# Performance work log

Hardware: AMD Instinct MI355X
Metric: run time of the kernel (lower is better)

The kernel has to match this reference:

```python
import jax, jax.numpy as jnp
import numpy as np

N = 200000      # nodes (Elliptic-scale transaction graph)
E = 400000      # directed edges
F_IN = 165      # node features
HID = 128
OUT = 2


def setup_inputs() -> dict:
    key = jax.random.key(0)
    k = jax.random.split(key, 5)
    x = jax.random.normal(k[0], (N, F_IN), dtype=jnp.float32)
    edge_index = jax.random.randint(k[1], (2, E), 0, N, dtype=jnp.int32)
    # GCNConv params (PyG: Linear without bias semantics differ slightly by
    # version; here weight + bias, bias added after aggregation)
    W1 = jax.random.normal(k[2], (F_IN, HID), dtype=jnp.float32) * (1.0 / np.sqrt(F_IN))
    b1 = jnp.zeros((HID,), dtype=jnp.float32)
    W2 = jax.random.normal(k[3], (HID, OUT), dtype=jnp.float32) * (1.0 / np.sqrt(HID))
    b2 = jnp.zeros((OUT,), dtype=jnp.float32)
    return {"x": x, "edge_index": edge_index, "W1": W1, "b1": b1, "W2": W2, "b2": b2}


def _gcn_conv(h, edge_index, W, b):
    """PyG GCNConv: out = D^{-1/2} (A + I) D^{-1/2} (h @ W) + b."""
    h = h @ W                                    # [N, F_out]
    loop = jnp.arange(N, dtype=edge_index.dtype)
    src = jnp.concatenate([edge_index[0], loop])  # add self-loops
    dst = jnp.concatenate([edge_index[1], loop])
    # degree over destination nodes (self-loops guarantee deg >= 1)
    deg = jax.ops.segment_sum(jnp.ones_like(dst, dtype=h.dtype), dst, num_segments=N)
    dinv = jax.lax.rsqrt(deg)
    norm = dinv[src] * dinv[dst]                 # [E+N]
    msgs = h[src] * norm[:, None]                # gather + scale
    out = jax.ops.segment_sum(msgs, dst, num_segments=N)  # scatter-add
    return out + b


def reference(x, edge_index, W1, b1, W2, b2):
    h = _gcn_conv(x, edge_index, W1, b1)
    # torch.relu then F.dropout(training=False) (identity) then torch.relu:
    # in eval mode relu(relu(h)) == relu(h)
    h = jnp.maximum(h, 0.0)
    return _gcn_conv(h, edge_index, W2, b2)
```

## Files before the change

### kernel.cpp

```cpp
#include <hip/hip_runtime.h>
#include <hip/hip_bf16.h>

typedef __attribute__((ext_vector_type(8))) short bf16x8;
typedef __attribute__((ext_vector_type(4))) float f32x4;

#define N_NODES 200000
#define N_EDGES 400000
#define F_IN    165
#define HID     128
#define BM      32
#define N_TILES 6250
#define KSTEPS  6
#define PITCH   164
#define CAP     32

__device__ __forceinline__ uint bf16r(float f) {
  uint u = __float_as_uint(f);
  return (u + 0x7FFFu + ((u >> 16) & 1u)) >> 16;
}

__device__ __forceinline__ uint pkbf(float a, float b) {
  uint r;
  asm("v_cvt_pk_bf16_f32 %0, %1, %2" : "=v"(r) : "v"(a), "v"(b));
  return r;
}

__device__ __forceinline__ void gload16(const void* gp, void* lp) {
  __builtin_amdgcn_global_load_lds(
      (const __attribute__((address_space(1))) unsigned int*)gp,
      (__attribute__((address_space(3))) unsigned int*)lp, 16, 0, 0);
}


__global__ __launch_bounds__(256) void k_init(const float* __restrict__ W1,
                                              ushort* __restrict__ Wf,
                                              uint4* __restrict__ cursor) {
  int b = blockIdx.x;
  int tid = threadIdx.x;
  if (b < 96) {
    int id = b * 256 + tid;
    int j = id & 7;
    int lane = (id >> 3) & 63;
    int rem = id >> 9;
    int s = rem % 6;
    int ct = rem / 6;
    int k = s * 32 + (lane >> 4) * 8 + j;
    int col = ct * 16 + (lane & 15);
    float v = (k < F_IN) ? W1[k * HID + col] : 0.f;
    Wf[id] = (ushort)bf16r(v);
  } else {
    int i = (b - 96) * 256 + tid;
    if (i < 50000) cursor[i] = make_uint4(0, 0, 0, 0);
  }
}


__global__ __launch_bounds__(256) void k_gemm1p(const float* __restrict__ x,
                                                const ushort* __restrict__ Wf,
                                                const int* __restrict__ ei,
                                                int* __restrict__ cursor,
                                                int* __restrict__ slots,
                                                uint* __restrict__ g) {
  __shared__ float xs[BM * PITCH + BM];
  float* xe = xs + BM * PITCH;
  const int tid  = threadIdx.x;
  const int wave = tid >> 6;
  const int lane = tid & 63;
  const int r15  = lane & 15;
  const int kg   = lane >> 4;

  if (tid < 64) {
    int e = blockIdx.x * 64 + tid;
    int d = ei[N_EDGES + e];
    int pos = atomicAdd(&cursor[d], 1);
    if (pos < CAP) slots[d * CAP + pos] = ei[e];
  }

  bf16x8 bfrag[2][KSTEPS];
  #pragma unroll
  for (int t = 0; t < 2; ++t) {
    int ct = wave * 2 + t;
    #pragma unroll
    for (int s = 0; s < KSTEPS; ++s)
      bfrag[t][s] = *(const bf16x8*)(Wf + (size_t)(((ct * KSTEPS + s) * 64 + lane) << 3));
  }

  const size_t tb = (size_t)blockIdx.x * (BM * F_IN);
  #pragma unroll
  for (int it = 0; it < 5; ++it) {
    int c = it * 256 + tid;
    int row = c / 41;
    int col4 = c - row * 41;
    gload16(x + tb + (size_t)row * F_IN + col4 * 4,
            (char*)xs + (size_t)(it * 256 + wave * 64) * 16);
  }
  if (tid < 32) {
    int c = 1280 + tid;
    int row = c / 41;
    int col4 = c - row * 41;
    float4 v;
    __builtin_memcpy(&v, x + tb + (size_t)row * F_IN + col4 * 4, 16);
    *(float4*)(xs + (size_t)c * 4) = v;
    xe[tid] = x[tb + (size_t)tid * F_IN + 164];
  }
  __syncthreads();

  f32x4 acc[2][2];
  #pragma unroll
  for (int rg = 0; rg < 2; ++rg) {
    acc[rg][0] = (f32x4){0.f, 0.f, 0.f, 0.f};
    acc[rg][1] = (f32x4){0.f, 0.f, 0.f, 0.f};
  }

  #pragma unroll
  for (int rg = 0; rg < 2; ++rg) {
    const float* rp0 = xs + (rg * 16 + r15) * PITCH;
    #pragma unroll
    for (int s = 0; s < KSTEPS; ++s) {
      uint o0, o1, o2, o3;
      if (s < 5) {
        const float* rp = rp0 + s * 32 + kg * 8;
        float4 fa = *(const float4*)rp;
        float4 fb = *(const float4*)(rp + 4);
        o0 = pkbf(fa.x, fa.y);
        o1 = pkbf(fa.z, fa.w);
        o2 = pkbf(fb.x, fb.y);
        o3 = pkbf(fb.z, fb.w);
      } else {
        o0 = o1 = o2 = o3 = 0u;
        if (kg == 0) {
          float4 fa = *(const float4*)(rp0 + 160);
          float e = xe[rg * 16 + r15];
          o0 = pkbf(fa.x, fa.y);
          o1 = pkbf(fa.z, fa.w);
          o2 = pkbf(e, 0.f);
        }
      }
      uint4 uu = make_uint4(o0, o1, o2, o3);
      bf16x8 a = *(bf16x8*)&uu;
      acc[rg][0] = __builtin_amdgcn_mfma_f32_16x16x32_bf16(a, bfrag[0][s], acc[rg][0], 0, 0, 0);
      acc[rg][1] = __builtin_amdgcn_mfma_f32_16x16x32_bf16(a, bfrag[1][s], acc[rg][1], 0, 0, 0);
    }
  }

  int base = blockIdx.x * BM;
  #pragma unroll
  for (int rg = 0; rg < 2; ++rg) {
    #pragma unroll
    for (int r = 0; r < 4; ++r) {
      int row = base + rg * 16 + kg * 4 + r;
      uint u = pkbf(acc[rg][0][r], acc[rg][1][r]);
      g[(size_t)row * 64 + wave * 16 + r15] = u;
    }
  }
}


__global__ __launch_bounds__(256, 8) void k_agg1(const uint* __restrict__ g,
                                                 const int* __restrict__ cursor,
                                                 const int* __restrict__ slots,
                                                 const float* __restrict__ b1,
                                                 const float* __restrict__ W2,
                                                 float* __restrict__ g2) {
  const int tid  = threadIdx.x;
  const int lane = tid & 63;
  const int wave = tid >> 6;
  const int sub  = lane >> 4;
  const int fl   = lane & 15;
  const int node = blockIdx.x * 16 + wave * 4 + sub;

  int deg = cursor[node];
  float dv = rsqrtf(1.0f + (float)deg);
  int dcap = min(deg, 16);
  int srcl = (fl < dcap) ? slots[node * CAP + fl] : node;

  uint4 v = *(const uint4*)&g[(size_t)node * 64 + fl * 4];
  float sx0 = dv * __uint_as_float(v.x << 16), sy0 = dv * __uint_as_float(v.x & 0xFFFF0000u);
  float sx1 = dv * __uint_as_float(v.y << 16), sy1 = dv * __uint_as_float(v.y & 0xFFFF0000u);
  float sx2 = dv * __uint_as_float(v.z << 16), sy2 = dv * __uint_as_float(v.z & 0xFFFF0000u);
  float sx3 = dv * __uint_as_float(v.w << 16), sy3 = dv * __uint_as_float(v.w & 0xFFFF0000u);

  for (int j = 0; j < dcap; ++j) {
    int s = __shfl(srcl, sub * 16 + j);
    float wj = rsqrtf(1.0f + (float)cursor[s]);
    uint4 w = *(const uint4*)&g[(size_t)s * 64 + fl * 4];
    sx0 = fmaf(__uint_as_float(w.x << 16), wj, sx0);
    sy0 = fmaf(__uint_as_float(w.x & 0xFFFF0000u), wj, sy0);
    sx1 = fmaf(__uint_as_float(w.y << 16), wj, sx1);
    sy1 = fmaf(__uint_as_float(w.y & 0xFFFF0000u), wj, sy1);
    sx2 = fmaf(__uint_as_float(w.z << 16), wj, sx2);
    sy2 = fmaf(__uint_as_float(w.z & 0xFFFF0000u), wj, sy2);
    sx3 = fmaf(__uint_as_float(w.w << 16), wj, sx3);
    sy3 = fmaf(__uint_as_float(w.w & 0xFFFF0000u), wj, sy3);
  }
  for (int e = 16; e < min(deg, CAP); ++e) {
    int s = slots[node * CAP + e];
    float wj = rsqrtf(1.0f + (float)cursor[s]);
    uint4 w = *(const uint4*)&g[(size_t)s * 64 + fl * 4];
    sx0 = fmaf(__uint_as_float(w.x << 16), wj, sx0);
    sy0 = fmaf(__uint_as_float(w.x & 0xFFFF0000u), wj, sy0);
    sx1 = fmaf(__uint_as_float(w.y << 16), wj, sx1);
    sy1 = fmaf(__uint_as_float(w.y & 0xFFFF0000u), wj, sy1);
    sx2 = fmaf(__uint_as_float(w.z << 16), wj, sx2);
    sy2 = fmaf(__uint_as_float(w.z & 0xFFFF0000u), wj, sy2);
    sx3 = fmaf(__uint_as_float(w.w << 16), wj, sx3);
    sy3 = fmaf(__uint_as_float(w.w & 0xFFFF0000u), wj, sy3);
  }

  float h, p0 = 0.f, p1 = 0.f;
  #pragma unroll
  for (int k = 0; k < 4; ++k) {
    int dw = fl * 4 + k;
    int c0 = ((dw >> 4) << 5) + (dw & 15);
    float blo = b1[c0], bhi = b1[c0 + 16];
    float2 wlo = *(const float2*)&W2[c0 * 2];
    float2 whi = *(const float2*)&W2[(c0 + 16) * 2];
    float sx = (k == 0) ? sx0 : (k == 1) ? sx1 : (k == 2) ? sx2 : sx3;
    float sy = (k == 0) ? sy0 : (k == 1) ? sy1 : (k == 2) ? sy2 : sy3;
    h = fmaxf(fmaf(sx, dv, blo), 0.f); p0 = fmaf(h, wlo.x, p0); p1 = fmaf(h, wlo.y, p1);
    h = fmaxf(fmaf(sy, dv, bhi), 0.f); p0 = fmaf(h, whi.x, p0); p1 = fmaf(h, whi.y, p1);
  }

  #pragma unroll
  for (int off = 1; off < 16; off <<= 1) {
    p0 += __shfl_xor(p0, off);
    p1 += __shfl_xor(p1, off);
  }
  if (fl == 0) {
    *(float2*)&g2[(size_t)node * 2] = make_float2(p0 * dv, p1 * dv);
  }
}


__global__ __launch_bounds__(256) void k_agg2(const float2* __restrict__ g2,
                                              const int* __restrict__ cursor,
                                              const int* __restrict__ slots,
                                              const float* __restrict__ b2,
                                              float* __restrict__ out) {
  int i = blockIdx.x * 256 + threadIdx.x;
  if (i >= N_NODES) return;
  float2 s = g2[i];
  int deg = cursor[i];
  int dcap = min(deg, CAP);
  for (int e = 0; e < dcap; ++e) {
    float2 m = g2[slots[i * CAP + e]];
    s.x += m.x;
    s.y += m.y;
  }
  float dv = rsqrtf(1.0f + (float)deg);
  float2 o;
  o.x = fmaf(s.x, dv, b2[0]);
  o.y = fmaf(s.y, dv, b2[1]);
  *(float2*)&out[(size_t)i * 2] = o;
}


extern "C" void kernel_launch(void* const* d_in, const int* in_sizes, int n_in,
                              void* d_out, int out_size, void* d_ws, size_t ws_size,
                              hipStream_t stream) {
  const float* x  = (const float*)d_in[0];
  const int*   ei = (const int*)d_in[1];
  const float* W1 = (const float*)d_in[2];
  const float* b1 = (const float*)d_in[3];
  const float* W2 = (const float*)d_in[4];
  const float* b2 = (const float*)d_in[5];
  float* out = (float*)d_out;

  char* ws = (char*)d_ws;
  size_t off = 0;
  auto take = [&](size_t bytes) -> char* {
    char* p = ws + off;
    off = (off + bytes + 255) & ~(size_t)255;
    return p;
  };
  int*    cursor = (int*)   take((size_t)N_NODES * 4);
  int*    slots  = (int*)   take((size_t)N_NODES * CAP * 4);
  float*  g2     = (float*) take((size_t)N_NODES * 2 * 4);
  ushort* Wf     = (ushort*)take((size_t)8 * KSTEPS * 64 * 8 * 2);
  uint*   g      = (uint*)  take((size_t)N_NODES * 64 * 4);
  (void)ws_size; (void)in_sizes; (void)n_in; (void)out_size;

  k_init<<<292, 256, 0, stream>>>(W1, Wf, (uint4*)cursor);
  k_gemm1p<<<N_TILES, 256, 0, stream>>>(x, Wf, ei, cursor, slots, g);
  k_agg1<<<12500, 256, 0, stream>>>(g, cursor, slots, b1, W2, g2);
  k_agg2<<<(N_NODES + 255) / 256, 256, 0, stream>>>((const float2*)g2, cursor,
                                                    slots, b2, out);
}
```

Baseline: 90.57 us.

## Sort nodes by degree bucket to balance aggregation warp work

Adds a histogram pass and a counting-sort permutation that groups nodes by in-degree, then has both aggregation kernels process nodes in that order. The goal is to cut divergence inside waves, where lanes handling low-degree nodes sit idle while others loop over many neighbours. The cost is two extra kernel launches and an indirect node lookup, and node outputs are now read and written in scattered order instead of contiguously.

New measurement: 113.9 us. +25.8%, slower.

```diff
diff --git a/kernel.cpp b/kernel.cpp
--- a/kernel.cpp
+++ b/kernel.cpp
@@ -13,6 +13,7 @@
 #define KSTEPS  6
 #define PITCH   164
 #define CAP     32
+#define NBLK    782
 
 __device__ __forceinline__ uint bf16r(float f) {
   uint u = __float_as_uint(f);
@@ -34,9 +35,11 @@
 
 __global__ __launch_bounds__(256) void k_init(const float* __restrict__ W1,
                                               ushort* __restrict__ Wf,
-                                              uint4* __restrict__ cursor) {
+                                              uint4* __restrict__ cursor,
+                                              int* __restrict__ bkt) {
   int b = blockIdx.x;
   int tid = threadIdx.x;
+  if (b == 0 && tid < 66) bkt[tid] = 0;
   if (b < 96) {
     int id = b * 256 + tid;
     int j = id & 7;
@@ -156,9 +159,47 @@
 }
 
 
+__global__ __launch_bounds__(256) void k_hist(const int* __restrict__ cursor,
+                                              int* __restrict__ bkt) {
+  __shared__ int h[33];
+  int tid = threadIdx.x;
+  if (tid < 33) h[tid] = 0;
+  __syncthreads();
+  int i = blockIdx.x * 256 + tid;
+  if (i < N_NODES) atomicAdd(&h[min(cursor[i], 32)], 1);
+  __syncthreads();
+  if (tid < 33 && h[tid]) atomicAdd(&bkt[tid], h[tid]);
+}
+
+
+__global__ __launch_bounds__(256) void k_perm(const int* __restrict__ cursor,
+                                              int* __restrict__ bkt,
+                                              int* __restrict__ perm) {
+  __shared__ int cnt[33], base[33], claim[33];
+  int tid = threadIdx.x;
+  if (tid < 33) cnt[tid] = 0;
+  __syncthreads();
+  int i = blockIdx.x * 256 + tid;
+  int bin = 0, r = 0;
+  if (i < N_NODES) {
+    bin = min(cursor[i], 32);
+    r = atomicAdd(&cnt[bin], 1);
+  }
+  __syncthreads();
+  if (tid == 0) {
+    int s = 0;
+    for (int k = 0; k < 33; ++k) { base[k] = s; s += bkt[k]; }
+  }
+  if (tid < 33) claim[tid] = cnt[tid] ? atomicAdd(&bkt[33 + tid], cnt[tid]) : 0;
+  __syncthreads();
+  if (i < N_NODES) perm[base[bin] + claim[bin] + r] = i;
+}
+
+
 __global__ __launch_bounds__(256, 8) void k_agg1(const uint* __restrict__ g,
                                                  const int* __restrict__ cursor,
                                                  const int* __restrict__ slots,
+                                                 const int* __restrict__ perm,
                                                  const float* __restrict__ b1,
                                                  const float* __restrict__ W2,
                                                  float* __restrict__ g2) {
@@ -167,7 +208,7 @@
   const int wave = tid >> 6;
   const int sub  = lane >> 4;
   const int fl   = lane & 15;
-  const int node = blockIdx.x * 16 + wave * 4 + sub;
+  const int node = perm[blockIdx.x * 16 + wave * 4 + sub];
 
   int deg = cursor[node];
   float dv = rsqrtf(1.0f + (float)deg);
@@ -235,10 +276,12 @@
 __global__ __launch_bounds__(256) void k_agg2(const float2* __restrict__ g2,
                                               const int* __restrict__ cursor,
                                               const int* __restrict__ slots,
+                                              const int* __restrict__ perm,
                                               const float* __restrict__ b2,
                                               float* __restrict__ out) {
-  int i = blockIdx.x * 256 + threadIdx.x;
-  if (i >= N_NODES) return;
+  int idx = blockIdx.x * 256 + threadIdx.x;
+  if (idx >= N_NODES) return;
+  int i = perm[idx];
   float2 s = g2[i];
   int deg = cursor[i];
   int dcap = min(deg, CAP);
@@ -275,14 +318,17 @@
   };
   int*    cursor = (int*)   take((size_t)N_NODES * 4);
   int*    slots  = (int*)   take((size_t)N_NODES * CAP * 4);
+  int*    bkt    = (int*)   take(66 * 4);
+  int*    perm   = (int*)   take((size_t)N_NODES * 4);
   float*  g2     = (float*) take((size_t)N_NODES * 2 * 4);
   ushort* Wf     = (ushort*)take((size_t)8 * KSTEPS * 64 * 8 * 2);
   uint*   g      = (uint*)  take((size_t)N_NODES * 64 * 4);
   (void)ws_size; (void)in_sizes; (void)n_in; (void)out_size;
 
-  k_init<<<292, 256, 0, stream>>>(W1, Wf, (uint4*)cursor);
+  k_init<<<292, 256, 0, stream>>>(W1, Wf, (uint4*)cursor, bkt);
   k_gemm1p<<<N_TILES, 256, 0, stream>>>(x, Wf, ei, cursor, slots, g);
-  k_agg1<<<12500, 256, 0, stream>>>(g, cursor, slots, b1, W2, g2);
-  k_agg2<<<(N_NODES + 255) / 256, 256, 0, stream>>>((const float2*)g2, cursor,
-                                                    slots, b2, out);
-}
+  k_hist<<<NBLK, 256, 0, stream>>>(cursor, bkt);
+  k_perm<<<NBLK, 256, 0, stream>>>(cursor, bkt, perm);
+  k_agg1<<<12500, 256, 0, stream>>>(g, cursor, slots, perm, b1, W2, g2);
+  k_agg2<<<NBLK, 256, 0, stream>>>((const float2*)g2, cursor, slots, perm, b2, out);
+}
```
